# Kernel tuning notes

Measured on AMD Instinct MI355X. Metric: run time of the kernel, lower is better.

Reference implementation:

```python
import jax, jax.numpy as jnp
import numpy as np

N_NODES = 50000
N_EDGES = 1600000
IN_C = 256
HID_C = 128
OUT_C = 16
HEADS = 8
NEG_SLOPE = 0.2  # PyG GATConv default


def gat_layer(x, src, dst, W, att_src, att_dst, bias, heads, out_c):
    """PyG-style GATConv (eval mode, add_self_loops already applied to src/dst).
    x: [N, F_in], W: [F_in, heads*out_c], att_*: [heads, out_c], bias: [heads*out_c].
    Returns concatenated heads: [N, heads*out_c]."""
    N = x.shape[0]
    h = (x @ W).reshape(N, heads, out_c)                  # [N, H, C]
    a_src = (h * att_src[None]).sum(-1)                   # [N, H]
    a_dst = (h * att_dst[None]).sum(-1)                   # [N, H]
    alpha = a_src[src] + a_dst[dst]                       # [E, H]
    alpha = jax.nn.leaky_relu(alpha, NEG_SLOPE)
    # segment softmax over incoming edges of each destination node
    amax = jax.ops.segment_max(alpha, dst, num_segments=N)  # [N, H]
    alpha = jnp.exp(alpha - jax.lax.stop_gradient(amax)[dst])
    denom = jax.ops.segment_sum(alpha, dst, num_segments=N)  # [N, H]
    w = alpha / denom[dst]                                # [E, H]
    msg = h[src] * w[:, :, None]                          # [E, H, C]
    out = jax.ops.segment_sum(msg, dst, num_segments=N)   # [N, H, C]
    return out.reshape(N, heads * out_c) + bias


def setup_inputs() -> dict:
    key = jax.random.key(0)
    ks = jax.random.split(key, 10)
    x = jax.random.normal(ks[0], (N_NODES, IN_C), dtype=jnp.float32)
    edge_index = jax.random.randint(ks[1], (2, N_EDGES), 0, N_NODES, dtype=jnp.int32)
    c1 = HID_C // HEADS  # 16 per head
    s1 = 1.0 / np.sqrt(IN_C)
    s2 = 1.0 / np.sqrt(HID_C)
    return {
        "x": x,
        "edge_index": edge_index,
        "W1": jax.random.normal(ks[2], (IN_C, HEADS * c1), dtype=jnp.float32) * s1,
        "att_src1": jax.random.normal(ks[3], (HEADS, c1), dtype=jnp.float32) * s1,
        "att_dst1": jax.random.normal(ks[4], (HEADS, c1), dtype=jnp.float32) * s1,
        "bias1": jnp.zeros((HEADS * c1,), dtype=jnp.float32),
        "W2": jax.random.normal(ks[5], (HID_C, OUT_C), dtype=jnp.float32) * s2,
        "att_src2": jax.random.normal(ks[6], (1, OUT_C), dtype=jnp.float32) * s2,
        "att_dst2": jax.random.normal(ks[7], (1, OUT_C), dtype=jnp.float32) * s2,
        "bias2": jnp.zeros((OUT_C,), dtype=jnp.float32),
    }


def reference(x, edge_index, W1, att_src1, att_dst1, bias1, W2, att_src2, att_dst2, bias2):
    N = x.shape[0]
    loop = jnp.arange(N, dtype=edge_index.dtype)
    src = jnp.concatenate([edge_index[0], loop])  # add_self_loops=True (PyG default)
    dst = jnp.concatenate([edge_index[1], loop])
    h = gat_layer(x, src, dst, W1, att_src1, att_dst1, bias1, HEADS, HID_C // HEADS)
    h = jax.nn.relu(h)
    # F.dropout with training=False is identity (eval mode)
    out = gat_layer(h, src, dst, W2, att_src2, att_dst2, bias2, 1, OUT_C)
    return out
```

## Files before the change

kernel.cpp:

```cpp
#include <hip/hip_runtime.h>
#include <hip/hip_bf16.h>


#define NN 50000
#define NE 1600000
#define NBK 196
#define NB_SC 512
#define CHUNK (NE / NB_SC)
#define GB1 782
#define GB2 1563

typedef __attribute__((ext_vector_type(8))) short bf16x8;
typedef __attribute__((ext_vector_type(4))) float f32x4;
typedef __attribute__((ext_vector_type(8))) _Float16 f16x8;
typedef __attribute__((ext_vector_type(8))) unsigned short u16x8;

__device__ __forceinline__ float lrelu(float x) { return fmaxf(x, 0.2f * x); }

__device__ __forceinline__ float ldf(const void* p, int i, int isbf) {
  return isbf ? __bfloat162float(((const __hip_bfloat16*)p)[i])
              : ((const float*)p)[i];
}
__device__ __forceinline__ short f2bf_bits(float v) {
  __hip_bfloat16 h = __float2bfloat16(v);
  return *reinterpret_cast<short*>(&h);
}
__device__ __forceinline__ unsigned short f2h_bits(float v) {
  _Float16 h = (_Float16)v;
  return *reinterpret_cast<unsigned short*>(&h);
}
__device__ __forceinline__ float f16lo(unsigned int u) {
  union { unsigned int u; _Float16 h[2]; } c; c.u = u; return (float)c.h[0];
}
__device__ __forceinline__ float f16hi(unsigned int u) {
  union { unsigned int u; _Float16 h[2]; } c; c.u = u; return (float)c.h[1];
}

#define OFF_H1   ((size_t)0)
#define OFF_H    ((size_t)25600000)
#define OFF_H2   ((size_t)51200000)
#define OFF_AS1  ((size_t)54400000)
#define OFF_AD1  ((size_t)56000000)
#define OFF_AS2  ((size_t)57600000)
#define OFF_AD2  ((size_t)57800000)
#define OFF_CNT  ((size_t)58000000)
#define OFF_OFFS ((size_t)58400000)
#define OFF_CSR  ((size_t)58600000)
#define OFF_WP1  ((size_t)65000000)
#define OFF_TOT  ((size_t)65065536)
#define OFF_FLAG ((size_t)65068608)

__global__ void repack_w1(const void* __restrict__ W1, short* __restrict__ Wp,
                          const unsigned int* __restrict__ xw, int* __restrict__ flag) {
  __shared__ int s[256];
  __shared__ int sf;
  int t = threadIdx.x;
  unsigned int w = xw[t * 97 + 5];
  unsigned int e = (w >> 7) & 0xFF;
  s[t] = (e >= 116 && e <= 138) ? 1 : 0;
  __syncthreads();
  for (int off = 128; off > 0; off >>= 1) {
    if (t < off) s[t] += s[t + off];
    __syncthreads();
  }
  if (t == 0) {
    sf = (s[0] >= 128) ? 1 : 0;
    if (blockIdx.x == 0) *flag = sf;
  }
  __syncthreads();
  int f = sf;
  int i = blockIdx.x * 256 + t;
  int j = i & 7, q = (i >> 3) & 3, c = (i >> 5) & 127, tt = i >> 12;
  int src = (tt * 32 + q * 8 + j) * 128 + c;
  Wp[i] = f ? ((const short*)W1)[src] : f2bf_bits(((const float*)W1)[src]);
}

__global__ __launch_bounds__(256) void fat1(const void* __restrict__ X,
                                            const short* __restrict__ Wp,
                                            unsigned short* __restrict__ H1h,
                                            const int* __restrict__ flag,
                                            const int* __restrict__ dst,
                                            int* __restrict__ HB) {
  __shared__ int h[224];
  if (blockIdx.x < GB1) {
    int wave = threadIdx.x >> 6, lane = threadIdx.x & 63;
    int rowbase = blockIdx.x * 64 + wave * 16;
    int l15 = lane & 15, quad = lane >> 4;
    int f = *flag;
    int arow = rowbase + l15;
    if (arow >= NN) arow = NN - 1;
    f32x4 acc[8];
#pragma unroll
    for (int ct = 0; ct < 8; ++ct) acc[ct] = (f32x4){0.f, 0.f, 0.f, 0.f};
    size_t abase = (size_t)arow * 256 + quad * 8;
#pragma unroll
    for (int kt = 0; kt < 8; ++kt) {
      bf16x8 a;
      if (f) {
        a = *(const bf16x8*)((const short*)X + abase + kt * 32);
      } else {
        const float* xp = (const float*)X + abase + kt * 32;
        float4 v0 = *(const float4*)xp, v1 = *(const float4*)(xp + 4);
        a[0] = f2bf_bits(v0.x); a[1] = f2bf_bits(v0.y);
        a[2] = f2bf_bits(v0.z); a[3] = f2bf_bits(v0.w);
        a[4] = f2bf_bits(v1.x); a[5] = f2bf_bits(v1.y);
        a[6] = f2bf_bits(v1.z); a[7] = f2bf_bits(v1.w);
      }
#pragma unroll
      for (int ct = 0; ct < 8; ++ct) {
        bf16x8 b = *(const bf16x8*)(Wp + ((kt * 128 + ct * 16 + l15) * 4 + quad) * 8);
        acc[ct] = __builtin_amdgcn_mfma_f32_16x16x32_bf16(a, b, acc[ct], 0, 0, 0);
      }
    }
    int r0 = rowbase + quad * 4;
#pragma unroll
    for (int ct = 0; ct < 8; ++ct)
#pragma unroll
      for (int r = 0; r < 4; ++r) {
        int row = r0 + r;
        if (row < NN) H1h[(size_t)row * 128 + ct * 16 + l15] = f2h_bits(acc[ct][r]);
      }
  } else {
    int b = blockIdx.x - GB1;
    int t = threadIdx.x;
    for (int i = t; i < 224; i += 256) h[i] = 0;
    __syncthreads();
    int e0 = b * CHUNK, e1 = e0 + CHUNK;
    for (int e = e0 + t; e < e1; e += 256) atomicAdd(&h[dst[e] >> 8], 1);
    __syncthreads();
    for (int i = t; i < NBK; i += 256) HB[b * NBK + i] = h[i];
  }
}

__global__ __launch_bounds__(256) void fat2(const unsigned short* __restrict__ H1h,
                                            const void* __restrict__ as1,
                                            const void* __restrict__ ad1,
                                            float* __restrict__ AS,
                                            float* __restrict__ AD,
                                            const int* __restrict__ flag,
                                            int* __restrict__ HB,
                                            int* __restrict__ total) {
  __shared__ float s_as[128], s_ad[128];
  __shared__ int ts[256];
  int t = threadIdx.x;
  if (blockIdx.x < GB2) {
    int f = *flag;
    if (t < 128) { s_as[t] = ldf(as1, t, f); s_ad[t] = ldf(ad1, t, f); }
    __syncthreads();
    int tid = blockIdx.x * 256 + t;
    if (tid >= NN * 8) return;
    int n = tid >> 3, hh = tid & 7;
    const f16x8* hp = (const f16x8*)(H1h + (size_t)n * 128 + hh * 16);
    f16x8 v0 = hp[0], v1 = hp[1];
    float as = 0.f, ad = 0.f;
#pragma unroll
    for (int i = 0; i < 8; ++i) {
      int b = hh * 16 + i;
      float x0 = (float)v0[i], x1 = (float)v1[i];
      as = fmaf(x0, s_as[b], fmaf(x1, s_as[b + 8], as));
      ad = fmaf(x0, s_ad[b], fmaf(x1, s_ad[b + 8], ad));
    }
    AS[tid] = as; AD[tid] = ad;
  } else {
    int k = blockIdx.x - GB2;
    int v0 = HB[(t * 2) * NBK + k], v1 = HB[(t * 2 + 1) * NBK + k];
    int s = v0 + v1;
    ts[t] = s;
    __syncthreads();
    for (int off = 1; off < 256; off <<= 1) {
      int a = (t >= off) ? ts[t - off] : 0;
      __syncthreads();
      ts[t] += a;
      __syncthreads();
    }
    int ex = ts[t] - s;
    HB[(t * 2) * NBK + k] = ex;
    HB[(t * 2 + 1) * NBK + k] = ex + v0;
    if (t == 255) total[k] = ts[255];
  }
}

__global__ __launch_bounds__(256) void scat_write(const int* __restrict__ src,
                                                  const int* __restrict__ dst,
                                                  const int* __restrict__ HB,
                                                  const int* __restrict__ total,
                                                  unsigned int* __restrict__ EPp) {
  __shared__ int h[224], sc[256], lofs[224], lc[224], gd[224];
  __shared__ unsigned int EB[CHUNK];
  __shared__ unsigned char BKT[CHUNK];
  int t = threadIdx.x, b = blockIdx.x;
  int tv = (t < NBK) ? total[t] : 0;
  sc[t] = tv;
  __syncthreads();
  for (int off = 1; off < 256; off <<= 1) {
    int a = (t >= off) ? sc[t - off] : 0;
    __syncthreads();
    sc[t] += a;
    __syncthreads();
  }
  if (t < NBK) gd[t] = (sc[t] - tv) + HB[b * NBK + t];
  for (int i = t; i < 224; i += 256) h[i] = 0;
  __syncthreads();
  int e0 = b * CHUNK, e1 = e0 + CHUNK;
  for (int e = e0 + t; e < e1; e += 256) atomicAdd(&h[dst[e] >> 8], 1);
  __syncthreads();
  int v = (t < NBK) ? h[t] : 0;
  sc[t] = v;
  __syncthreads();
  for (int off = 1; off < 256; off <<= 1) {
    int a = (t >= off) ? sc[t - off] : 0;
    __syncthreads();
    sc[t] += a;
    __syncthreads();
  }
  if (t < NBK) { int ex = sc[t] - v; lofs[t] = ex; lc[t] = ex; }
  __syncthreads();
  for (int e = e0 + t; e < e1; e += 256) {
    int d = dst[e];
    int k = d >> 8;
    int pos = atomicAdd(&lc[k], 1);
    EB[pos] = ((unsigned int)(d & 255) << 16) | (unsigned int)src[e];
    BKT[pos] = (unsigned char)k;
  }
  __syncthreads();
  for (int pos = t; pos < CHUNK; pos += 256) {
    int k = BKT[pos];
    EPp[gd[k] + (pos - lofs[k])] = EB[pos];
  }
}

__global__ __launch_bounds__(1024) void bucket_csr(const unsigned int* __restrict__ EPp,
                                                   const int* __restrict__ total,
                                                   int* __restrict__ cnt,
                                                   int* __restrict__ offs,
                                                   unsigned short* __restrict__ csr) {
  __shared__ int h[256], sc[256], lc[256];
  int b = blockIdx.x, t = threadIdx.x;
  int tv = 0;
  if (t < 256) { tv = (t < NBK) ? total[t] : 0; sc[t] = tv; }
  __syncthreads();
  for (int off = 1; off < 256; off <<= 1) {
    int a = (t >= off && t < 256) ? sc[t - off] : 0;
    __syncthreads();
    if (t < 256) sc[t] += a;
    __syncthreads();
  }
  __shared__ int s_gbase, s_n;
  if (t == (unsigned)b) { s_gbase = sc[b] - tv; s_n = tv; }
  __syncthreads();
  int gbase = s_gbase, n = s_n;
  if (t < 256) h[t] = 0;
  __syncthreads();
  for (int i = t; i < n; i += 1024) atomicAdd(&h[(EPp[gbase + i] >> 16) & 255], 1);
  __syncthreads();
  int v = 0;
  if (t < 256) { v = h[t]; sc[t] = v; }
  __syncthreads();
  for (int off = 1; off < 256; off <<= 1) {
    int add = (t >= off && t < 256) ? sc[t - off] : 0;
    __syncthreads();
    if (t < 256) sc[t] += add;
    __syncthreads();
  }
  if (t < 256) {
    int ex = sc[t] - v;
    int node = (b << 8) + t;
    if (node < NN) { cnt[node] = v; offs[node] = gbase + ex; }
    lc[t] = ex;
  }
  __syncthreads();
  for (int i = t; i < n; i += 1024) {
    unsigned int p = EPp[gbase + i];
    int pos = atomicAdd(&lc[(p >> 16) & 255], 1);
    csr[gbase + pos] = (unsigned short)(p & 0xFFFF);
  }
}

__global__ __launch_bounds__(256) void agg1(const unsigned short* __restrict__ H1h,
                                            const float* __restrict__ AS,
                                            const float* __restrict__ AD,
                                            const int* __restrict__ offs,
                                            const int* __restrict__ cnt,
                                            const unsigned short* __restrict__ csr,
                                            const void* __restrict__ bias1,
                                            unsigned short* __restrict__ Hh,
                                            const int* __restrict__ flag) {
  int lane = threadIdx.x & 63;
  int node = blockIdx.x * 4 + (threadIdx.x >> 6);
  int f = *flag;
  int start = offs[node], deg = cnt[node];
  int g = lane >> 3, k = lane & 7;
  float adst = AD[node * 8 + k];
  float acc[16];
#pragma unroll
  for (int i = 0; i < 16; ++i) acc[i] = 0.f;
  float dsum = 0.f;
  if (g == 0) {
    float p = __expf(lrelu(AS[node * 8 + k] + adst));
    dsum = p;
    const f16x8* hp = (const f16x8*)(H1h + (size_t)node * 128 + k * 16);
    f16x8 v0 = hp[0], v1 = hp[1];
#pragma unroll
    for (int i = 0; i < 8; ++i) {
      acc[i] = fmaf(p, (float)v0[i], acc[i]);
      acc[8 + i] = fmaf(p, (float)v1[i], acc[8 + i]);
    }
  }
  int s0 = (g < deg) ? (int)csr[start + g] : -1;
  float a0 = 0.f; f16x8 u0a, u0b;
  if (s0 >= 0) {
    a0 = AS[s0 * 8 + k];
    const f16x8* hp = (const f16x8*)(H1h + (size_t)s0 * 128 + k * 16);
    u0a = hp[0]; u0b = hp[1];
  }
  int s1 = (8 + g < deg) ? (int)csr[start + 8 + g] : -1;
  for (int eb = 0; eb < deg; eb += 8) {
    float a1 = 0.f; f16x8 u1a, u1b;
    if (s1 >= 0) {
      a1 = AS[s1 * 8 + k];
      const f16x8* hp = (const f16x8*)(H1h + (size_t)s1 * 128 + k * 16);
      u1a = hp[0]; u1b = hp[1];
    }
    int en2 = eb + 16 + g;
    int s2 = (en2 < deg) ? (int)csr[start + en2] : -1;
    if (s0 >= 0) {
      float p = __expf(lrelu(a0 + adst));
      dsum += p;
#pragma unroll
      for (int i = 0; i < 8; ++i) {
        acc[i] = fmaf(p, (float)u0a[i], acc[i]);
        acc[8 + i] = fmaf(p, (float)u0b[i], acc[8 + i]);
      }
    }
    s0 = s1; a0 = a1; u0a = u1a; u0b = u1b; s1 = s2;
  }
#pragma unroll
  for (int i = 0; i < 16; ++i) {
    acc[i] += __shfl_xor(acc[i], 8);
    acc[i] += __shfl_xor(acc[i], 16);
    acc[i] += __shfl_xor(acc[i], 32);
  }
  dsum += __shfl_xor(dsum, 8);
  dsum += __shfl_xor(dsum, 16);
  dsum += __shfl_xor(dsum, 32);
  if (g == 0) {
    float inv = 1.0f / dsum;
    int c0 = k * 16;
    u16x8 o0, o1;
#pragma unroll
    for (int i = 0; i < 8; ++i) {
      o0[i] = f2h_bits(fmaxf(acc[i] * inv + ldf(bias1, c0 + i, f), 0.f));
      o1[i] = f2h_bits(fmaxf(acc[8 + i] * inv + ldf(bias1, c0 + 8 + i, f), 0.f));
    }
    *(u16x8*)(Hh + (size_t)node * 128 + c0) = o0;
    *(u16x8*)(Hh + (size_t)node * 128 + c0 + 8) = o1;
  }
}

__global__ __launch_bounds__(256) void gemm2_a2(const unsigned short* __restrict__ Hb,
                                                const void* __restrict__ W2,
                                                const void* __restrict__ as2,
                                                const void* __restrict__ ad2,
                                                unsigned short* __restrict__ H2h,
                                                float* __restrict__ AS2,
                                                float* __restrict__ AD2,
                                                const int* __restrict__ flag) {
  __shared__ float sW[2048];
  __shared__ float s_as[16], s_ad[16];
  int t = threadIdx.x;
  int f = *flag;
  for (int i = t; i < 2048; i += 256) sW[i] = ldf(W2, i, f);
  if (t < 16) { s_as[t] = ldf(as2, t, f); s_ad[t] = ldf(ad2, t, f); }
  __syncthreads();
  int n = blockIdx.x * 16 + (t >> 4), c = t & 15;
  const f16x8* hp = (const f16x8*)(Hb + (size_t)n * 128);
  float acc = 0.f;
#pragma unroll 4
  for (int k8 = 0; k8 < 16; ++k8) {
    f16x8 v = hp[k8];
#pragma unroll
    for (int i = 0; i < 8; ++i) acc = fmaf((float)v[i], sW[(k8 * 8 + i) * 16 + c], acc);
  }
  H2h[n * 16 + c] = f2h_bits(acc);
  float vs = acc * s_as[c], vd = acc * s_ad[c];
#pragma unroll
  for (int off = 1; off < 16; off <<= 1) {
    vs += __shfl_xor(vs, off);
    vd += __shfl_xor(vd, off);
  }
  if (c == 0) { AS2[n] = vs; AD2[n] = vd; }
}

__global__ __launch_bounds__(256) void agg2(const unsigned short* __restrict__ H2h,
                                            const float* __restrict__ AS2,
                                            const float* __restrict__ AD2,
                                            const int* __restrict__ offs,
                                            const int* __restrict__ cnt,
                                            const unsigned short* __restrict__ csr,
                                            const void* __restrict__ bias2,
                                            void* __restrict__ outv,
                                            const int* __restrict__ flag) {
  int lane = threadIdx.x & 63;
  int node = blockIdx.x * 4 + (threadIdx.x >> 6);
  int f = *flag;
  int start = offs[node], deg = cnt[node];
  int g = lane >> 3, k = lane & 7;
  float adst = AD2[node];
  float a0 = 0.f, a1 = 0.f, dsum = 0.f;
  if (g == 0) {
    float p = __expf(lrelu(AS2[node] + adst));
    dsum = p;
    unsigned int hv = *(const unsigned int*)(H2h + (size_t)node * 16 + k * 2);
    a0 = fmaf(p, f16lo(hv), a0);
    a1 = fmaf(p, f16hi(hv), a1);
  }
  int s0 = (g < deg) ? (int)csr[start + g] : -1;
  float as_c = 0.f; unsigned int hv_c = 0;
  if (s0 >= 0) {
    as_c = AS2[s0];
    hv_c = *(const unsigned int*)(H2h + (size_t)s0 * 16 + k * 2);
  }
  int s1 = (8 + g < deg) ? (int)csr[start + 8 + g] : -1;
  for (int eb = 0; eb < deg; eb += 8) {
    float as_n = 0.f; unsigned int hv_n = 0;
    if (s1 >= 0) {
      as_n = AS2[s1];
      hv_n = *(const unsigned int*)(H2h + (size_t)s1 * 16 + k * 2);
    }
    int en2 = eb + 16 + g;
    int s2 = (en2 < deg) ? (int)csr[start + en2] : -1;
    if (s0 >= 0) {
      float p = __expf(lrelu(as_c + adst));
      dsum += p;
      a0 = fmaf(p, f16lo(hv_c), a0);
      a1 = fmaf(p, f16hi(hv_c), a1);
    }
    s0 = s1; as_c = as_n; hv_c = hv_n; s1 = s2;
  }
  a0 += __shfl_xor(a0, 8);  a0 += __shfl_xor(a0, 16);  a0 += __shfl_xor(a0, 32);
  a1 += __shfl_xor(a1, 8);  a1 += __shfl_xor(a1, 16);  a1 += __shfl_xor(a1, 32);
  dsum += __shfl_xor(dsum, 8); dsum += __shfl_xor(dsum, 16); dsum += __shfl_xor(dsum, 32);
  if (g == 0) {
    float inv = 1.0f / dsum;
    float o0 = a0 * inv + ldf(bias2, k * 2 + 0, f);
    float o1 = a1 * inv + ldf(bias2, k * 2 + 1, f);
    size_t base = (size_t)node * 16 + k * 2;
    if (f) {
      ((__hip_bfloat16*)outv)[base] = __float2bfloat16(o0);
      ((__hip_bfloat16*)outv)[base + 1] = __float2bfloat16(o1);
    } else {
      *(float2*)((float*)outv + base) = make_float2(o0, o1);
    }
  }
}

extern "C" void kernel_launch(void* const* d_in, const int* in_sizes, int n_in,
                              void* d_out, int out_size, void* d_ws, size_t ws_size,
                              hipStream_t stream) {
  const void* x = d_in[0];
  const int* ei = (const int*)d_in[1];
  const void* W1 = d_in[2];
  const void* as1 = d_in[3];
  const void* ad1 = d_in[4];
  const void* b1 = d_in[5];
  const void* W2 = d_in[6];
  const void* as2 = d_in[7];
  const void* ad2 = d_in[8];
  const void* b2 = d_in[9];
  char* ws = (char*)d_ws;

  unsigned short* H1h = (unsigned short*)(ws + OFF_H1);
  unsigned short* Hh = (unsigned short*)(ws + OFF_H);
  unsigned int* EPp = (unsigned int*)(ws + OFF_H);
  unsigned short* H2h = (unsigned short*)(ws + OFF_H2);
  int* HB = (int*)(ws + OFF_H2);
  float* AS1 = (float*)(ws + OFF_AS1);
  float* AD1 = (float*)(ws + OFF_AD1);
  float* AS2 = (float*)(ws + OFF_AS2);
  float* AD2 = (float*)(ws + OFF_AD2);
  int* CNT = (int*)(ws + OFF_CNT);
  int* OFFS = (int*)(ws + OFF_OFFS);
  unsigned short* CSR = (unsigned short*)(ws + OFF_CSR);
  short* Wp = (short*)(ws + OFF_WP1);
  int* TOT = (int*)(ws + OFF_TOT);
  int* FLAG = (int*)(ws + OFF_FLAG);

  repack_w1<<<128, 256, 0, stream>>>(W1, Wp, (const unsigned int*)x, FLAG);
  fat1<<<GB1 + NB_SC, 256, 0, stream>>>(x, Wp, H1h, FLAG, ei + NE, HB);
  fat2<<<GB2 + NBK, 256, 0, stream>>>(H1h, as1, ad1, AS1, AD1, FLAG, HB, TOT);
  scat_write<<<NB_SC, 256, 0, stream>>>(ei, ei + NE, HB, TOT, EPp);
  bucket_csr<<<NBK, 1024, 0, stream>>>(EPp, TOT, CNT, OFFS, CSR);

  agg1<<<NN / 4, 256, 0, stream>>>(H1h, AS1, AD1, OFFS, CNT, CSR, b1, Hh, FLAG);
  gemm2_a2<<<NN / 16, 256, 0, stream>>>(Hh, W2, as2, ad2, H2h, AS2, AD2, FLAG);
  agg2<<<NN / 4, 256, 0, stream>>>(H2h, AS2, AD2, OFFS, CNT, CSR, b2, d_out, FLAG);
}
```

Baseline: 265.5 us.

## Fuse attention logits into GEMM1 epilogue and layer-2 GEMM into agg1

The per-node attention scores for layer 1 are now computed in the fat1 MFMA epilogue from the fp32 accumulators, using shuffle reductions, so H1 no longer has to be re-read in a separate pass. The bucket scan becomes its own small kernel. agg1 now applies bias and ReLU and then immediately multiplies by W2 (staged in LDS) to produce H2 and the layer-2 attention scores. This removes the intermediate 128-wide hidden tensor write/read and the gemm2 launch. In exchange, every agg1 block now loads W2 into LDS and does extra shuffle and FMA work.

```diff
diff --git a/kernel.cpp b/kernel.cpp
--- a/kernel.cpp
+++ b/kernel.cpp
@@ -8,7 +8,6 @@
 #define NB_SC 512
 #define CHUNK (NE / NB_SC)
 #define GB1 782
-#define GB2 1563
 
 typedef __attribute__((ext_vector_type(8))) short bf16x8;
 typedef __attribute__((ext_vector_type(4))) float f32x4;
@@ -80,13 +79,21 @@
                                             unsigned short* __restrict__ H1h,
                                             const int* __restrict__ flag,
                                             const int* __restrict__ dst,
-                                            int* __restrict__ HB) {
+                                            int* __restrict__ HB,
+                                            const void* __restrict__ as1,
+                                            const void* __restrict__ ad1,
+                                            float* __restrict__ AS,
+                                            float* __restrict__ AD) {
   __shared__ int h[224];
+  __shared__ float s_as1[128], s_ad1[128];
   if (blockIdx.x < GB1) {
-    int wave = threadIdx.x >> 6, lane = threadIdx.x & 63;
+    int t = threadIdx.x;
+    int wave = t >> 6, lane = t & 63;
     int rowbase = blockIdx.x * 64 + wave * 16;
     int l15 = lane & 15, quad = lane >> 4;
     int f = *flag;
+    if (t < 128) { s_as1[t] = ldf(as1, t, f); s_ad1[t] = ldf(ad1, t, f); }
+    __syncthreads();
     int arow = rowbase + l15;
     if (arow >= NN) arow = NN - 1;
     f32x4 acc[8];
@@ -120,6 +127,31 @@
         int row = r0 + r;
         if (row < NN) H1h[(size_t)row * 128 + ct * 16 + l15] = f2h_bits(acc[ct][r]);
       }
+    float hs[4], hd[4];
+#pragma unroll
+    for (int r = 0; r < 4; ++r) { hs[r] = 0.f; hd[r] = 0.f; }
+#pragma unroll
+    for (int ct = 0; ct < 8; ++ct) {
+      float sa = s_as1[ct * 16 + l15], sd = s_ad1[ct * 16 + l15];
+#pragma unroll
+      for (int r = 0; r < 4; ++r) {
+        float vs = acc[ct][r] * sa;
+        float vd = acc[ct][r] * sd;
+        vs += __shfl_xor(vs, 1); vd += __shfl_xor(vd, 1);
+        vs += __shfl_xor(vs, 2); vd += __shfl_xor(vd, 2);
+        vs += __shfl_xor(vs, 4); vd += __shfl_xor(vd, 4);
+        vs += __shfl_xor(vs, 8); vd += __shfl_xor(vd, 8);
+        if (l15 == ct) { hs[r] = vs; hd[r] = vd; }
+      }
+    }
+#pragma unroll
+    for (int r = 0; r < 4; ++r) {
+      int row = r0 + r;
+      if (l15 < 8 && row < NN) {
+        AS[row * 8 + l15] = hs[r];
+        AD[row * 8 + l15] = hd[r];
+      }
+    }
   } else {
     int b = blockIdx.x - GB1;
     int t = threadIdx.x;
@@ -132,52 +164,25 @@
   }
 }
 
-__global__ __launch_bounds__(256) void fat2(const unsigned short* __restrict__ H1h,
-                                            const void* __restrict__ as1,
-                                            const void* __restrict__ ad1,
-                                            float* __restrict__ AS,
-                                            float* __restrict__ AD,
-                                            const int* __restrict__ flag,
-                                            int* __restrict__ HB,
-                                            int* __restrict__ total) {
-  __shared__ float s_as[128], s_ad[128];
+__global__ __launch_bounds__(256) void scan1(int* __restrict__ HB,
+                                             int* __restrict__ total) {
   __shared__ int ts[256];
   int t = threadIdx.x;
-  if (blockIdx.x < GB2) {
-    int f = *flag;
-    if (t < 128) { s_as[t] = ldf(as1, t, f); s_ad[t] = ldf(ad1, t, f); }
-    __syncthreads();
-    int tid = blockIdx.x * 256 + t;
-    if (tid >= NN * 8) return;
-    int n = tid >> 3, hh = tid & 7;
-    const f16x8* hp = (const f16x8*)(H1h + (size_t)n * 128 + hh * 16);
-    f16x8 v0 = hp[0], v1 = hp[1];
-    float as = 0.f, ad = 0.f;
-#pragma unroll
-    for (int i = 0; i < 8; ++i) {
-      int b = hh * 16 + i;
-      float x0 = (float)v0[i], x1 = (float)v1[i];
-      as = fmaf(x0, s_as[b], fmaf(x1, s_as[b + 8], as));
-      ad = fmaf(x0, s_ad[b], fmaf(x1, s_ad[b + 8], ad));
-    }
-    AS[tid] = as; AD[tid] = ad;
-  } else {
-    int k = blockIdx.x - GB2;
-    int v0 = HB[(t * 2) * NBK + k], v1 = HB[(t * 2 + 1) * NBK + k];
-    int s = v0 + v1;
-    ts[t] = s;
-    __syncthreads();
-    for (int off = 1; off < 256; off <<= 1) {
-      int a = (t >= off) ? ts[t - off] : 0;
-      __syncthreads();
-      ts[t] += a;
-      __syncthreads();
-    }
-    int ex = ts[t] - s;
-    HB[(t * 2) * NBK + k] = ex;
-    HB[(t * 2 + 1) * NBK + k] = ex + v0;
-    if (t == 255) total[k] = ts[255];
-  }
+  int k = blockIdx.x;
+  int v0 = HB[(t * 2) * NBK + k], v1 = HB[(t * 2 + 1) * NBK + k];
+  int s = v0 + v1;
+  ts[t] = s;
+  __syncthreads();
+  for (int off = 1; off < 256; off <<= 1) {
+    int a = (t >= off) ? ts[t - off] : 0;
+    __syncthreads();
+    ts[t] += a;
+    __syncthreads();
+  }
+  int ex = ts[t] - s;
+  HB[(t * 2) * NBK + k] = ex;
+  HB[(t * 2 + 1) * NBK + k] = ex + v0;
+  if (t == 255) total[k] = ts[255];
 }
 
 __global__ __launch_bounds__(256) void scat_write(const int* __restrict__ src,
@@ -283,11 +288,26 @@
                                             const int* __restrict__ cnt,
                                             const unsigned short* __restrict__ csr,
                                             const void* __restrict__ bias1,
-                                            unsigned short* __restrict__ Hh,
+                                            const void* __restrict__ W2,
+                                            const void* __restrict__ as2,
+                                            const void* __restrict__ ad2,
+                                            unsigned short* __restrict__ H2h,
+                                            float* __restrict__ AS2,
+                                            float* __restrict__ AD2,
                                             const int* __restrict__ flag) {
-  int lane = threadIdx.x & 63;
-  int node = blockIdx.x * 4 + (threadIdx.x >> 6);
+  __shared__ float sW2p[8 * 264];
+  __shared__ float s_b1[128], s_a2[16], s_d2[16];
+  int t = threadIdx.x;
   int f = *flag;
+  for (int idx = t; idx < 2048; idx += 256) {
+    int ch = idx >> 4, c = idx & 15, kk = ch >> 4, ii = ch & 15;
+    sW2p[kk * 264 + ii * 16 + c] = ldf(W2, idx, f);
+  }
+  if (t < 128) s_b1[t] = ldf(bias1, t, f);
+  if (t < 16) { s_a2[t] = ldf(as2, t, f); s_d2[t] = ldf(ad2, t, f); }
+  __syncthreads();
+  int lane = t & 63;
+  int node = blockIdx.x * 4 + (t >> 6);
   int start = offs[node], deg = cnt[node];
   int g = lane >> 3, k = lane & 7;
   float adst = AD[node * 8 + k];
@@ -343,52 +363,33 @@
   dsum += __shfl_xor(dsum, 8);
   dsum += __shfl_xor(dsum, 16);
   dsum += __shfl_xor(dsum, 32);
-  if (g == 0) {
-    float inv = 1.0f / dsum;
-    int c0 = k * 16;
-    u16x8 o0, o1;
-#pragma unroll
-    for (int i = 0; i < 8; ++i) {
-      o0[i] = f2h_bits(fmaxf(acc[i] * inv + ldf(bias1, c0 + i, f), 0.f));
-      o1[i] = f2h_bits(fmaxf(acc[8 + i] * inv + ldf(bias1, c0 + 8 + i, f), 0.f));
-    }
-    *(u16x8*)(Hh + (size_t)node * 128 + c0) = o0;
-    *(u16x8*)(Hh + (size_t)node * 128 + c0 + 8) = o1;
-  }
-}
-
-__global__ __launch_bounds__(256) void gemm2_a2(const unsigned short* __restrict__ Hb,
-                                                const void* __restrict__ W2,
-                                                const void* __restrict__ as2,
-                                                const void* __restrict__ ad2,
-                                                unsigned short* __restrict__ H2h,
-                                                float* __restrict__ AS2,
-                                                float* __restrict__ AD2,
-                                                const int* __restrict__ flag) {
-  __shared__ float sW[2048];
-  __shared__ float s_as[16], s_ad[16];
-  int t = threadIdx.x;
-  int f = *flag;
-  for (int i = t; i < 2048; i += 256) sW[i] = ldf(W2, i, f);
-  if (t < 16) { s_as[t] = ldf(as2, t, f); s_ad[t] = ldf(ad2, t, f); }
-  __syncthreads();
-  int n = blockIdx.x * 16 + (t >> 4), c = t & 15;
-  const f16x8* hp = (const f16x8*)(Hb + (size_t)n * 128);
-  float acc = 0.f;
-#pragma unroll 4
-  for (int k8 = 0; k8 < 16; ++k8) {
-    f16x8 v = hp[k8];
-#pragma unroll
-    for (int i = 0; i < 8; ++i) acc = fmaf((float)v[i], sW[(k8 * 8 + i) * 16 + c], acc);
-  }
-  H2h[n * 16 + c] = f2h_bits(acc);
-  float vs = acc * s_as[c], vd = acc * s_ad[c];
-#pragma unroll
-  for (int off = 1; off < 16; off <<= 1) {
-    vs += __shfl_xor(vs, off);
-    vd += __shfl_xor(vd, off);
-  }
-  if (c == 0) { AS2[n] = vs; AD2[n] = vd; }
+  float inv = 1.0f / dsum;
+  float rowv[16];
+#pragma unroll
+  for (int i = 0; i < 16; ++i)
+    rowv[i] = fmaxf(acc[i] * inv + s_b1[k * 16 + i], 0.f);
+  float h2a = 0.f, h2b = 0.f;
+  const float* wbase = &sW2p[k * 264 + 2 * g];
+#pragma unroll
+  for (int i = 0; i < 16; ++i) {
+    float2 w = *(const float2*)(wbase + i * 16);
+    h2a = fmaf(rowv[i], w.x, h2a);
+    h2b = fmaf(rowv[i], w.y, h2b);
+  }
+  h2a += __shfl_xor(h2a, 1); h2b += __shfl_xor(h2b, 1);
+  h2a += __shfl_xor(h2a, 2); h2b += __shfl_xor(h2b, 2);
+  h2a += __shfl_xor(h2a, 4); h2b += __shfl_xor(h2b, 4);
+  if (k == 0) {
+    unsigned int pk = (unsigned int)(unsigned short)f2h_bits(h2a)
+                    | ((unsigned int)(unsigned short)f2h_bits(h2b) << 16);
+    *(unsigned int*)(H2h + (size_t)node * 16 + 2 * g) = pk;
+  }
+  float vs = h2a * s_a2[2 * g] + h2b * s_a2[2 * g + 1];
+  float vd = h2a * s_d2[2 * g] + h2b * s_d2[2 * g + 1];
+  vs += __shfl_xor(vs, 8); vd += __shfl_xor(vd, 8);
+  vs += __shfl_xor(vs, 16); vd += __shfl_xor(vd, 16);
+  vs += __shfl_xor(vs, 32); vd += __shfl_xor(vd, 32);
+  if (lane == 0) { AS2[node] = vs; AD2[node] = vd; }
 }
 
 __global__ __launch_bounds__(256) void agg2(const unsigned short* __restrict__ H2h,
@@ -470,7 +471,6 @@
   char* ws = (char*)d_ws;
 
   unsigned short* H1h = (unsigned short*)(ws + OFF_H1);
-  unsigned short* Hh = (unsigned short*)(ws + OFF_H);
   unsigned int* EPp = (unsigned int*)(ws + OFF_H);
   unsigned short* H2h = (unsigned short*)(ws + OFF_H2);
   int* HB = (int*)(ws + OFF_H2);
@@ -486,12 +486,13 @@
   int* FLAG = (int*)(ws + OFF_FLAG);
 
   repack_w1<<<128, 256, 0, stream>>>(W1, Wp, (const unsigned int*)x, FLAG);
-  fat1<<<GB1 + NB_SC, 256, 0, stream>>>(x, Wp, H1h, FLAG, ei + NE, HB);
-  fat2<<<GB2 + NBK, 256, 0, stream>>>(H1h, as1, ad1, AS1, AD1, FLAG, HB, TOT);
+  fat1<<<GB1 + NB_SC, 256, 0, stream>>>(x, Wp, H1h, FLAG, ei + NE, HB,
+                                        as1, ad1, AS1, AD1);
+  scan1<<<NBK, 256, 0, stream>>>(HB, TOT);
   scat_write<<<NB_SC, 256, 0, stream>>>(ei, ei + NE, HB, TOT, EPp);
   bucket_csr<<<NBK, 1024, 0, stream>>>(EPp, TOT, CNT, OFFS, CSR);
 
-  agg1<<<NN / 4, 256, 0, stream>>>(H1h, AS1, AD1, OFFS, CNT, CSR, b1, Hh, FLAG);
-  gemm2_a2<<<NN / 16, 256, 0, stream>>>(Hh, W2, as2, ad2, H2h, AS2, AD2, FLAG);
+  agg1<<<NN / 4, 256, 0, stream>>>(H1h, AS1, AD1, OFFS, CNT, CSR, b1,
+                                   W2, as2, ad2, H2h, AS2, AD2, FLAG);
   agg2<<<NN / 4, 256, 0, stream>>>(H2h, AS2, AD2, OFFS, CNT, CSR, b2, d_out, FLAG);
 }
```

Result: no change. 270.5 us (+1.9%).

## Fuse layer-2 projection and attention logits into agg1 epilogue

Applied to the files above, without the earlier changes.

The separate gemm2_a2 kernel is removed. agg1 now applies bias and ReLU and then computes the 128x16 W2 projection plus the layer-2 attention logits directly from its register accumulators, spreading the work across lanes with shuffles. This drops one kernel launch and the write and re-read of the 50000x128 fp16 hidden activations. In exchange, every wave reads W2 from global or cache memory instead of shared memory, the epilogue gains more shuffles, and the accumulators are packed as float2 vectors, which may allow packed FMA.

```diff
diff --git a/kernel.cpp b/kernel.cpp
--- a/kernel.cpp
+++ b/kernel.cpp
@@ -12,6 +12,7 @@
 
 typedef __attribute__((ext_vector_type(8))) short bf16x8;
 typedef __attribute__((ext_vector_type(4))) float f32x4;
+typedef __attribute__((ext_vector_type(2))) float f32x2;
 typedef __attribute__((ext_vector_type(8))) _Float16 f16x8;
 typedef __attribute__((ext_vector_type(8))) unsigned short u16x8;
 
@@ -20,6 +21,16 @@
 __device__ __forceinline__ float ldf(const void* p, int i, int isbf) {
   return isbf ? __bfloat162float(((const __hip_bfloat16*)p)[i])
               : ((const float*)p)[i];
+}
+__device__ __forceinline__ f32x2 ldf2(const void* p, int i, int isbf) {
+  if (isbf) {
+    unsigned int u = *(const unsigned int*)((const unsigned short*)p + i);
+    union { unsigned int u; float f; } lo, hi;
+    lo.u = u << 16;
+    hi.u = u & 0xFFFF0000u;
+    return (f32x2){lo.f, hi.f};
+  }
+  return *(const f32x2*)((const float*)p + i);
 }
 __device__ __forceinline__ short f2bf_bits(float v) {
   __hip_bfloat16 h = __float2bfloat16(v);
@@ -283,7 +294,12 @@
                                             const int* __restrict__ cnt,
                                             const unsigned short* __restrict__ csr,
                                             const void* __restrict__ bias1,
-                                            unsigned short* __restrict__ Hh,
+                                            const void* __restrict__ W2,
+                                            const void* __restrict__ as2,
+                                            const void* __restrict__ ad2,
+                                            unsigned short* __restrict__ H2h,
+                                            float* __restrict__ AS2,
+                                            float* __restrict__ AD2,
                                             const int* __restrict__ flag) {
   int lane = threadIdx.x & 63;
   int node = blockIdx.x * 4 + (threadIdx.x >> 6);
@@ -291,19 +307,22 @@
   int start = offs[node], deg = cnt[node];
   int g = lane >> 3, k = lane & 7;
   float adst = AD[node * 8 + k];
-  float acc[16];
-#pragma unroll
-  for (int i = 0; i < 16; ++i) acc[i] = 0.f;
+  f32x2 acc2[8];
+#pragma unroll
+  for (int j = 0; j < 8; ++j) acc2[j] = (f32x2){0.f, 0.f};
   float dsum = 0.f;
   if (g == 0) {
     float p = __expf(lrelu(AS[node * 8 + k] + adst));
     dsum = p;
     const f16x8* hp = (const f16x8*)(H1h + (size_t)node * 128 + k * 16);
     f16x8 v0 = hp[0], v1 = hp[1];
-#pragma unroll
-    for (int i = 0; i < 8; ++i) {
-      acc[i] = fmaf(p, (float)v0[i], acc[i]);
-      acc[8 + i] = fmaf(p, (float)v1[i], acc[8 + i]);
+    f32x2 p2 = (f32x2){p, p};
+#pragma unroll
+    for (int j = 0; j < 4; ++j) {
+      f32x2 xa = (f32x2){(float)v0[2 * j], (float)v0[2 * j + 1]};
+      f32x2 xb = (f32x2){(float)v1[2 * j], (float)v1[2 * j + 1]};
+      acc2[j] = xa * p2 + acc2[j];
+      acc2[4 + j] = xb * p2 + acc2[4 + j];
     }
   }
   int s0 = (g < deg) ? (int)csr[start + g] : -1;
@@ -326,69 +345,59 @@
     if (s0 >= 0) {
       float p = __expf(lrelu(a0 + adst));
       dsum += p;
-#pragma unroll
-      for (int i = 0; i < 8; ++i) {
-        acc[i] = fmaf(p, (float)u0a[i], acc[i]);
-        acc[8 + i] = fmaf(p, (float)u0b[i], acc[8 + i]);
+      f32x2 p2 = (f32x2){p, p};
+#pragma unroll
+      for (int j = 0; j < 4; ++j) {
+        f32x2 xa = (f32x2){(float)u0a[2 * j], (float)u0a[2 * j + 1]};
+        f32x2 xb = (f32x2){(float)u0b[2 * j], (float)u0b[2 * j + 1]};
+        acc2[j] = xa * p2 + acc2[j];
+        acc2[4 + j] = xb * p2 + acc2[4 + j];
       }
     }
     s0 = s1; a0 = a1; u0a = u1a; u0b = u1b; s1 = s2;
   }
 #pragma unroll
-  for (int i = 0; i < 16; ++i) {
-    acc[i] += __shfl_xor(acc[i], 8);
-    acc[i] += __shfl_xor(acc[i], 16);
-    acc[i] += __shfl_xor(acc[i], 32);
+  for (int j = 0; j < 8; ++j) {
+    acc2[j].x += __shfl_xor(acc2[j].x, 8);
+    acc2[j].y += __shfl_xor(acc2[j].y, 8);
+    acc2[j].x += __shfl_xor(acc2[j].x, 16);
+    acc2[j].y += __shfl_xor(acc2[j].y, 16);
+    acc2[j].x += __shfl_xor(acc2[j].x, 32);
+    acc2[j].y += __shfl_xor(acc2[j].y, 32);
   }
   dsum += __shfl_xor(dsum, 8);
   dsum += __shfl_xor(dsum, 16);
   dsum += __shfl_xor(dsum, 32);
-  if (g == 0) {
-    float inv = 1.0f / dsum;
-    int c0 = k * 16;
-    u16x8 o0, o1;
-#pragma unroll
-    for (int i = 0; i < 8; ++i) {
-      o0[i] = f2h_bits(fmaxf(acc[i] * inv + ldf(bias1, c0 + i, f), 0.f));
-      o1[i] = f2h_bits(fmaxf(acc[8 + i] * inv + ldf(bias1, c0 + 8 + i, f), 0.f));
-    }
-    *(u16x8*)(Hh + (size_t)node * 128 + c0) = o0;
-    *(u16x8*)(Hh + (size_t)node * 128 + c0 + 8) = o1;
-  }
-}
-
-__global__ __launch_bounds__(256) void gemm2_a2(const unsigned short* __restrict__ Hb,
-                                                const void* __restrict__ W2,
-                                                const void* __restrict__ as2,
-                                                const void* __restrict__ ad2,
-                                                unsigned short* __restrict__ H2h,
-                                                float* __restrict__ AS2,
-                                                float* __restrict__ AD2,
-                                                const int* __restrict__ flag) {
-  __shared__ float sW[2048];
-  __shared__ float s_as[16], s_ad[16];
-  int t = threadIdx.x;
-  int f = *flag;
-  for (int i = t; i < 2048; i += 256) sW[i] = ldf(W2, i, f);
-  if (t < 16) { s_as[t] = ldf(as2, t, f); s_ad[t] = ldf(ad2, t, f); }
-  __syncthreads();
-  int n = blockIdx.x * 16 + (t >> 4), c = t & 15;
-  const f16x8* hp = (const f16x8*)(Hb + (size_t)n * 128);
-  float acc = 0.f;
-#pragma unroll 4
-  for (int k8 = 0; k8 < 16; ++k8) {
-    f16x8 v = hp[k8];
-#pragma unroll
-    for (int i = 0; i < 8; ++i) acc = fmaf((float)v[i], sW[(k8 * 8 + i) * 16 + c], acc);
-  }
-  H2h[n * 16 + c] = f2h_bits(acc);
-  float vs = acc * s_as[c], vd = acc * s_ad[c];
-#pragma unroll
-  for (int off = 1; off < 16; off <<= 1) {
-    vs += __shfl_xor(vs, off);
-    vd += __shfl_xor(vd, off);
-  }
-  if (c == 0) { AS2[n] = vs; AD2[n] = vd; }
+  float inv = 1.0f / dsum;
+#pragma unroll
+  for (int j = 0; j < 8; ++j) {
+    f32x2 b = ldf2(bias1, k * 16 + 2 * j, f);
+    acc2[j].x = fmaxf(acc2[j].x * inv + b.x, 0.f);
+    acc2[j].y = fmaxf(acc2[j].y * inv + b.y, 0.f);
+  }
+  float h2x = 0.f, h2y = 0.f;
+#pragma unroll
+  for (int i = 0; i < 16; ++i) {
+    float rv = (i & 1) ? acc2[i >> 1].y : acc2[i >> 1].x;
+    f32x2 w = ldf2(W2, (k * 16 + i) * 16 + 2 * g, f);
+    h2x = fmaf(rv, w.x, h2x);
+    h2y = fmaf(rv, w.y, h2y);
+  }
+  h2x += __shfl_xor(h2x, 1); h2y += __shfl_xor(h2y, 1);
+  h2x += __shfl_xor(h2x, 2); h2y += __shfl_xor(h2y, 2);
+  h2x += __shfl_xor(h2x, 4); h2y += __shfl_xor(h2y, 4);
+  if (k == 0) {
+    unsigned int pk = (unsigned int)(unsigned short)f2h_bits(h2x)
+                    | ((unsigned int)(unsigned short)f2h_bits(h2y) << 16);
+    *(unsigned int*)(H2h + (size_t)node * 16 + 2 * g) = pk;
+  }
+  f32x2 sa = ldf2(as2, 2 * g, f), sd = ldf2(ad2, 2 * g, f);
+  float vs = h2x * sa.x + h2y * sa.y;
+  float vd = h2x * sd.x + h2y * sd.y;
+  vs += __shfl_xor(vs, 8);  vd += __shfl_xor(vd, 8);
+  vs += __shfl_xor(vs, 16); vd += __shfl_xor(vd, 16);
+  vs += __shfl_xor(vs, 32); vd += __shfl_xor(vd, 32);
+  if (lane == 0) { AS2[node] = vs; AD2[node] = vd; }
 }
 
 __global__ __launch_bounds__(256) void agg2(const unsigned short* __restrict__ H2h,
@@ -470,7 +479,6 @@
   char* ws = (char*)d_ws;
 
   unsigned short* H1h = (unsigned short*)(ws + OFF_H1);
-  unsigned short* Hh = (unsigned short*)(ws + OFF_H);
   unsigned int* EPp = (unsigned int*)(ws + OFF_H);
   unsigned short* H2h = (unsigned short*)(ws + OFF_H2);
   int* HB = (int*)(ws + OFF_H2);
@@ -491,7 +499,7 @@
   scat_write<<<NB_SC, 256, 0, stream>>>(ei, ei + NE, HB, TOT, EPp);
   bucket_csr<<<NBK, 1024, 0, stream>>>(EPp, TOT, CNT, OFFS, CSR);
 
-  agg1<<<NN / 4, 256, 0, stream>>>(H1h, AS1, AD1, OFFS, CNT, CSR, b1, Hh, FLAG);
-  gemm2_a2<<<NN / 16, 256, 0, stream>>>(Hh, W2, as2, ad2, H2h, AS2, AD2, FLAG);
+  agg1<<<NN / 4, 256, 0, stream>>>(H1h, AS1, AD1, OFFS, CNT, CSR, b1,
+                                   W2, as2, ad2, H2h, AS2, AD2, FLAG);
   agg2<<<NN / 4, 256, 0, stream>>>(H2h, AS2, AD2, OFFS, CNT, CSR, b2, d_out, FLAG);
 }
```

Result: slower. 342.5 us (+29.0%).
